# Kernel optimization log

Hardware: AMD Instinct MI355X
Metric: run time of the kernel (lower is better)

The kernel has to match this reference:

```python
import jax, jax.numpy as jnp
import numpy as np

B, T, V, LSRC, D = 4, 128, 50257, 512, 512
PAD_ID = 0
GAMMA1, GAMMA2 = 1.0, 0.1
BETA, MAX_ITER = 2.0, 400


def setup_inputs() -> dict:
    key = jax.random.key(0)
    ks = jax.random.split(key, 7)
    # output_mle are per-token probabilities (original takes torch.log of them)
    output_mle = jax.random.uniform(ks[0], (B, T, V), jnp.float32, 1e-4, 1.0)
    attn_dist = jax.random.uniform(ks[1], (B, LSRC, T), jnp.float32)
    coverage = jax.random.uniform(ks[2], (B, LSRC, T), jnp.float32)
    trg = jax.random.randint(ks[3], (B, T), 0, V)
    dec_mask = jax.random.randint(ks[4], (B, T), 0, 2).astype(bool)
    dec_len = jax.random.randint(ks[5], (B,), 1, T)
    W_emb = jax.random.normal(ks[6], (V, D), jnp.float32) * 0.02
    return {"output_mle": output_mle, "attn_dist": attn_dist, "coverage": coverage,
            "trg": trg, "dec_mask": dec_mask, "dec_len": dec_len, "W_emb": W_emb}


def ipot(a1, a2, beta=BETA, max_iter=MAX_ITER):
    # a1, a2: [n, d_hid] (already flattened from [B, T, d_hid])
    n = a1.shape[0]
    a1n = a1 / jnp.linalg.norm(a1, axis=1, keepdims=True)
    a2n = a2 / jnp.linalg.norm(a2, axis=1, keepdims=True)
    C = a1n @ a2n.T                      # [n, n] cosine cost
    A = jnp.exp(-C / beta)
    eye = jnp.eye(n, dtype=C.dtype)
    sigma0 = jnp.full((n, 1), 1.0 / n, C.dtype)
    T0 = jnp.full((n, n), 1.0 / (n * n), C.dtype)

    def step(carry, _):
        Tm, sigma = carry
        Q = A * Tm
        dvec = 1.0 / n / (Q @ sigma)          # [n, 1]
        sigma = 1.0 / n / (Q.T @ dvec)        # [n, 1]
        # Faithful to torch source: diag(d) * Q * diag(sigma) is ELEMENTWISE,
        # so only the diagonal of the product survives.
        Tm = dvec * Q * sigma.T * eye
        return (Tm, sigma), None

    (Tm, _), _ = jax.lax.scan(step, (T0, sigma0), None, length=max_iter)
    return jnp.sum(Tm * C)


def reference(output_mle, attn_dist, coverage, trg, dec_mask, dec_len, W_emb):
    # --- NLL loss (Eq. 6): mean -log p[target] over non-pad tokens ---
    logp = jnp.log(output_mle)
    tok_lp = jnp.take_along_axis(logp, trg[..., None], axis=-1)[..., 0]   # [B, T]
    valid = (trg != PAD_ID)
    nll = -jnp.sum(jnp.where(valid, tok_lp, 0.0)) / jnp.sum(valid).astype(logp.dtype)

    # --- Coverage loss (Eq. 12) ---
    cov = jnp.sum(jnp.minimum(attn_dist, coverage), axis=1)               # [B, T]
    cov = jnp.where(dec_mask, 0.0, cov)
    cov_loss = jnp.sum(cov) / jnp.sum(dec_len).astype(cov.dtype)

    # --- OT loss via IPOT ---
    trg_emb = W_emb[trg]                                                  # [B, T, D]
    probs = jax.nn.softmax(output_mle, axis=-1)
    pred = jnp.einsum('btv,vd->btd', probs, W_emb)                        # [B, T, D]
    ot = ipot(pred.reshape(-1, D), trg_emb.reshape(-1, D))

    # Faithful to source: gamma2 added as a constant (not multiplied by ot)
    return nll + GAMMA1 * cov_loss + GAMMA2 + ot
```

## Files before the change

### kernel.cpp

```cpp
#include <hip/hip_runtime.h>
#include <math.h>

#define B_ 4
#define T_ 128
#define V_ 50257
#define D_ 512
#define NROWS 512
#define GAMMA2_ 0.1f

#define BK 32
#define KC 1600
#define SPLITK 32
#define NIT (KC / BK)
#define LDA 40
#define LDB 40
#define SLICE (NROWS * D_)
#define WS_PART_OFF 1024

#define SPLITK2 48
#define KC2 1056
#define KP 50688
#define NXB 2048
#define NWB ((KP / 64) * (D_ / 64))
#define ACC_BYTES 4096
#define XB_BYTES ((size_t)NROWS * KP * 2)
#define WT_BYTES ((size_t)D_ * KP * 2)
#define PART2_BYTES ((size_t)SPLITK2 * SLICE * 4)
#define NEED_NEW (ACC_BYTES + XB_BYTES + WT_BYTES + PART2_BYTES)

typedef __attribute__((ext_vector_type(8))) short s8v;
typedef __attribute__((ext_vector_type(4))) float f4v;

__device__ inline unsigned int pack2bf(float f0, float f1) {
    unsigned int u0 = __float_as_uint(f0);
    unsigned int u1 = __float_as_uint(f1);
    u0 += 0x7fffu + ((u0 >> 16) & 1u);
    u1 += 0x7fffu + ((u1 >> 16) & 1u);
    return (u0 >> 16) | (u1 & 0xffff0000u);
}

__device__ inline void sync_lds() {
    __builtin_amdgcn_s_waitcnt(0xC07F);
    __builtin_amdgcn_s_barrier();
}

__device__ inline float wave_reduce(float v) {
    #pragma unroll
    for (int o = 32; o > 0; o >>= 1) v += __shfl_down(v, o, 64);
    return v;
}

__device__ __forceinline__ void gload16(const unsigned short* g, unsigned short* l) {
    __builtin_amdgcn_global_load_lds(
        (const __attribute__((address_space(1))) unsigned int*)g,
        (__attribute__((address_space(3))) unsigned int*)l, 16, 0, 0);
}

__device__ void misc_body(int bid,
                          const float* __restrict__ output_mle,
                          const float* __restrict__ attn,
                          const float* __restrict__ cover,
                          const int* __restrict__ trg,
                          const int* __restrict__ dec_mask,
                          const int* __restrict__ dec_len,
                          float* __restrict__ acc) {
    if (bid < 64) {
        float s = 0.f;
        const float4* a4 = (const float4*)attn;
        const float4* c4 = (const float4*)cover;
        for (int i4 = bid * 256 + threadIdx.x; i4 < 65536; i4 += 64 * 256) {
            float4 a = a4[i4];
            float4 c = c4[i4];
            int b = i4 >> 14;
            int t = (i4 << 2) & (T_ - 1);
            int4 m = *(const int4*)&dec_mask[(b << 7) + t];
            s += m.x ? 0.f : fminf(a.x, c.x);
            s += m.y ? 0.f : fminf(a.y, c.y);
            s += m.z ? 0.f : fminf(a.z, c.z);
            s += m.w ? 0.f : fminf(a.w, c.w);
        }
        s = wave_reduce(s);
        if ((threadIdx.x & 63) == 0) atomicAdd(&acc[2], s);
    } else {
        float lp = 0.f, cnt = 0.f;
        for (int i = threadIdx.x; i < NROWS; i += 256) {
            int tg = trg[i];
            if (tg != 0) {
                lp += __logf(output_mle[(size_t)i * V_ + tg]);
                cnt += 1.f;
            }
        }
        lp = wave_reduce(lp); cnt = wave_reduce(cnt);
        if ((threadIdx.x & 63) == 0) { atomicAdd(&acc[0], lp); atomicAdd(&acc[1], cnt); }
        if (threadIdx.x < B_) atomicAdd(&acc[3], (float)dec_len[threadIdx.x]);
    }
}

__global__ void misc_kernel(const float* __restrict__ output_mle,
                            const float* __restrict__ attn,
                            const float* __restrict__ cover,
                            const int* __restrict__ trg,
                            const int* __restrict__ dec_mask,
                            const int* __restrict__ dec_len,
                            float* __restrict__ acc) {
    misc_body(blockIdx.x, output_mle, attn, cover, trg, dec_mask, dec_len, acc);
}

__launch_bounds__(256)
__global__ void prep_kernel(const float* __restrict__ X,
                            const float* __restrict__ W,
                            const float* __restrict__ attn,
                            const float* __restrict__ cover,
                            const int* __restrict__ trg,
                            const int* __restrict__ dec_mask,
                            const int* __restrict__ dec_len,
                            float* __restrict__ acc,
                            unsigned short* __restrict__ Xb,
                            unsigned short* __restrict__ Wt) {
    const int bid = blockIdx.x;
    const int tid = threadIdx.x;
    if (bid < NXB) {
        const int upr = KP / 8;
        for (int u = bid * 256 + tid; u < NROWS * upr; u += NXB * 256) {
            int row = u / upr;
            int k8  = (u - row * upr) * 8;
            const float* src = X + (size_t)row * V_ + k8;
            unsigned int pk[4];
            if (k8 + 8 <= V_) {
                float e[8];
                #pragma unroll
                for (int j = 0; j < 8; j++) e[j] = __expf(src[j]);
                #pragma unroll
                for (int p = 0; p < 4; p++) pk[p] = pack2bf(e[2 * p], e[2 * p + 1]);
            } else {
                #pragma unroll
                for (int p = 0; p < 4; p++) {
                    float e0 = (k8 + 2 * p     < V_) ? __expf(src[2 * p])     : 0.f;
                    float e1 = (k8 + 2 * p + 1 < V_) ? __expf(src[2 * p + 1]) : 0.f;
                    pk[p] = pack2bf(e0, e1);
                }
            }
            *(uint4*)&Xb[(size_t)row * KP + k8] = *(uint4*)pk;
        }
    } else if (bid < NXB + NWB) {
        __shared__ float Ls[64][64];
        int w  = bid - NXB;
        int kt = w >> 3;
        int dt = w & 7;
        int k0 = kt << 6, d0 = dt << 6;
        int r0 = tid >> 4;
        int c0 = (tid & 15) << 2;
        #pragma unroll
        for (int q = 0; q < 4; q++) {
            int r  = (q << 4) + r0;
            int gk = k0 + r;
            float4 v;
            if (gk < V_) v = *(const float4*)&W[(size_t)gk * D_ + d0 + c0];
            else         v = make_float4(0.f, 0.f, 0.f, 0.f);
            *(float4*)&Ls[r][c0] = v;
        }
        __syncthreads();
        int d  = tid >> 2;
        int kc = (tid & 3) << 4;
        unsigned int pk[8];
        #pragma unroll
        for (int p = 0; p < 8; p++)
            pk[p] = pack2bf(Ls[kc + 2 * p][d], Ls[kc + 2 * p + 1][d]);
        unsigned short* dst = Wt + (size_t)(d0 + d) * KP + k0 + kc;
        *(uint4*)&dst[0] = *(uint4*)&pk[0];
        *(uint4*)&dst[8] = *(uint4*)&pk[4];
    } else {
        misc_body(bid - (NXB + NWB), X, attn, cover, trg, dec_mask, dec_len, acc);
    }
}

__launch_bounds__(256)
__global__ void gemm2_kernel(const unsigned short* __restrict__ Xb,
                             const unsigned short* __restrict__ Wt,
                             float* __restrict__ part) {
    __shared__ __align__(16) unsigned short As[128 * 32];
    __shared__ __align__(16) unsigned short Bs[128 * 32];

    const int bx   = blockIdx.x;
    const int tile = bx & 15;
    const int s    = bx >> 4;
    const int i0   = (tile & 3) * 128;
    const int d0   = (tile >> 2) * 128;
    const size_t ks = (size_t)s * KC2;

    const int tid  = threadIdx.x;
    const int lane = tid & 63;
    const int wave = tid >> 6;
    const int wm   = (wave & 1) * 64;
    const int wn   = (wave >> 1) * 64;
    const int l15  = lane & 15;
    const int l4   = lane >> 4;

    const int grow = wave * 16 + (lane >> 2);
    const int gk8  = (lane & 3) * 8;
    const unsigned short* gA0 = Xb + (size_t)(i0 + grow) * KP + ks + gk8;
    const unsigned short* gA1 = gA0 + (size_t)64 * KP;
    const unsigned short* gB0 = Wt + (size_t)(d0 + grow) * KP + ks + gk8;
    const unsigned short* gB1 = gB0 + (size_t)64 * KP;
    unsigned short* lA = As + wave * 512;
    unsigned short* lB = Bs + wave * 512;

    f4v acc[4][4];
    #pragma unroll
    for (int a = 0; a < 4; a++)
        #pragma unroll
        for (int b = 0; b < 4; b++) acc[a][b] = (f4v)0.f;

    #pragma unroll 1
    for (int kk = 0; kk < KC2; kk += 32) {
        __syncthreads();
        gload16(gA0 + kk, lA);
        gload16(gA1 + kk, lA + 2048);
        gload16(gB0 + kk, lB);
        gload16(gB1 + kk, lB + 2048);
        __syncthreads();
        s8v af[4], bfr[4];
        #pragma unroll
        for (int mi = 0; mi < 4; mi++)
            af[mi] = *(const s8v*)&As[(wm + mi * 16 + l15) * 32 + l4 * 8];
        #pragma unroll
        for (int ni = 0; ni < 4; ni++)
            bfr[ni] = *(const s8v*)&Bs[(wn + ni * 16 + l15) * 32 + l4 * 8];
        #pragma unroll
        for (int mi = 0; mi < 4; mi++)
            #pragma unroll
            for (int ni = 0; ni < 4; ni++)
                acc[mi][ni] = __builtin_amdgcn_mfma_f32_16x16x32_bf16(
                    af[mi], bfr[ni], acc[mi][ni], 0, 0, 0);
    }

    float* dst = part + (size_t)s * SLICE;
    #pragma unroll
    for (int mi = 0; mi < 4; mi++) {
        #pragma unroll
        for (int ni = 0; ni < 4; ni++) {
            int col = d0 + wn + ni * 16 + l15;
            #pragma unroll
            for (int r = 0; r < 4; r++) {
                int row = i0 + wm + mi * 16 + l4 * 4 + r;
                dst[row * D_ + col] = acc[mi][ni][r];
            }
        }
    }
}

__launch_bounds__(256)
__global__ void gemm_kernel(const float* __restrict__ X,
                            const float* __restrict__ W,
                            float* __restrict__ part,
                            int use_atomic) {
    __shared__ __align__(16) short As[128 * LDA];
    __shared__ __align__(16) short Bs[128 * LDB];

    const int bx   = blockIdx.x;
    const int tile = bx & 15;
    const int s    = bx >> 4;
    const int i0   = (tile & 3) * 128;
    const int d0   = (tile >> 2) * 128;
    const int ks   = s * KC;
    const int ke   = min(ks + KC, V_);

    const int tid  = threadIdx.x;
    const int lane = tid & 63;
    const int wave = tid >> 6;
    const int wm   = (wave & 1) * 64;
    const int wn   = (wave >> 1) * 64;
    const int l15  = lane & 15;
    const int l4   = lane >> 4;

    const int ar   = tid >> 1;
    const int akh  = (tid & 1) * 16;
    const int bn2  = (tid & 63) * 2;
    const int bkq  = (tid >> 6) * 8;

    f4v acc[4][4];
    #pragma unroll
    for (int a = 0; a < 4; a++)
        #pragma unroll
        for (int b = 0; b < 4; b++) acc[a][b] = (f4v)0.f;

    auto stageA = [&](const float4 (&ab)[4]) {
        const float* f = (const float*)&ab[0];
        unsigned int au[8];
        #pragma unroll
        for (int p = 0; p < 8; p++)
            au[p] = pack2bf(__expf(f[2 * p]), __expf(f[2 * p + 1]));
        *(uint4*)&As[ar * LDA + akh]     = *(const uint4*)&au[0];
        *(uint4*)&As[ar * LDA + akh + 8] = *(const uint4*)&au[4];
    };
    auto stageB = [&](const float2 (&bb)[8]) {
        unsigned int r0[4], r1[4];
        #pragma unroll
        for (int p = 0; p < 4; p++) {
            r0[p] = pack2bf(bb[2 * p].x, bb[2 * p + 1].x);
            r1[p] = pack2bf(bb[2 * p].y, bb[2 * p + 1].y);
        }
        *(uint4*)&Bs[bn2 * LDB + bkq]       = *(const uint4*)&r0[0];
        *(uint4*)&Bs[(bn2 + 1) * LDB + bkq] = *(const uint4*)&r1[0];
    };
    auto domfma = [&]() {
        s8v af[4], bfr[4];
        #pragma unroll
        for (int mi = 0; mi < 4; mi++)
            af[mi] = *(const s8v*)&As[(wm + mi * 16 + l15) * LDA + l4 * 8];
        #pragma unroll
        for (int ni = 0; ni < 4; ni++)
            bfr[ni] = *(const s8v*)&Bs[(wn + ni * 16 + l15) * LDB + l4 * 8];
        #pragma unroll
        for (int mi = 0; mi < 4; mi++)
            #pragma unroll
            for (int ni = 0; ni < 4; ni++)
                acc[mi][ni] = __builtin_amdgcn_mfma_f32_16x16x32_bf16(
                    af[mi], bfr[ni], acc[mi][ni], 0, 0, 0);
    };
    auto issue = [&](float4 (&ab)[4], float2 (&bb)[8], const float* ap, const float* bp) {
        #pragma unroll
        for (int q = 0; q < 4; q++) ab[q] = *(const float4*)(ap + q * 4);
        #pragma unroll
        for (int j = 0; j < 8; j++) bb[j] = *(const float2*)(bp + (size_t)j * D_);
    };

    if (ks + KC <= V_) {
        const float* ap = X + (size_t)(i0 + ar) * V_ + ks + akh;
        const float* bp = W + d0 + bn2 + (size_t)(ks + bkq) * D_;
        float4 a0[4], a1[4];
        float2 b0[8], b1[8];
        issue(a0, b0, ap, bp);
        #pragma unroll 1
        for (int it = 0; it < NIT; it += 2) {
            ap += BK; bp += (size_t)BK * D_;
            if (it + 1 < NIT) issue(a1, b1, ap, bp);
            sync_lds();
            stageA(a0); stageB(b0);
            sync_lds();
            domfma();

            ap += BK; bp += (size_t)BK * D_;
            if (it + 2 < NIT) issue(a0, b0, ap, bp);
            sync_lds();
            stageA(a1); stageB(b1);
            sync_lds();
            domfma();
        }
    } else {
        const float* Abase = X + (size_t)(i0 + ar) * V_;
        const float* Bbase = W + d0 + bn2;
        for (int k0 = ks; k0 < ke; k0 += BK) {
            float4 ab[4];
            float2 bb[8];
            #pragma unroll
            for (int q = 0; q < 4; q++) {
                int gk = min(k0 + akh + q * 4, V_ - 4);
                ab[q] = *(const float4*)(Abase + gk);
            }
            #pragma unroll
            for (int j = 0; j < 8; j++) {
                int gk = min(k0 + bkq + j, V_ - 1);
                bb[j] = *(const float2*)(Bbase + (size_t)gk * D_);
            }
            sync_lds();
            {
                unsigned int au[8];
                const float* f = (const float*)&ab[0];
                #pragma unroll
                for (int p = 0; p < 8; p++) {
                    int g0 = k0 + akh + 2 * p;
                    float e0 = (g0     < ke) ? __expf(f[2 * p])     : 0.f;
                    float e1 = (g0 + 1 < ke) ? __expf(f[2 * p + 1]) : 0.f;
                    au[p] = pack2bf(e0, e1);
                }
                *(uint4*)&As[ar * LDA + akh]     = *(const uint4*)&au[0];
                *(uint4*)&As[ar * LDA + akh + 8] = *(const uint4*)&au[4];
            }
            {
                unsigned int r0[4], r1[4];
                #pragma unroll
                for (int p = 0; p < 4; p++) {
                    int g0 = k0 + bkq + 2 * p;
                    float x0 = (g0     < ke) ? bb[2 * p].x     : 0.f;
                    float x1 = (g0 + 1 < ke) ? bb[2 * p + 1].x : 0.f;
                    float y0 = (g0     < ke) ? bb[2 * p].y     : 0.f;
                    float y1 = (g0 + 1 < ke) ? bb[2 * p + 1].y : 0.f;
                    r0[p] = pack2bf(x0, x1);
                    r1[p] = pack2bf(y0, y1);
                }
                *(uint4*)&Bs[bn2 * LDB + bkq]       = *(const uint4*)&r0[0];
                *(uint4*)&Bs[(bn2 + 1) * LDB + bkq] = *(const uint4*)&r1[0];
            }
            sync_lds();
            domfma();
        }
    }

    float* dst = part + (use_atomic ? 0 : (size_t)s * SLICE);
    #pragma unroll
    for (int mi = 0; mi < 4; mi++) {
        #pragma unroll
        for (int ni = 0; ni < 4; ni++) {
            int col = d0 + wn + ni * 16 + l15;
            #pragma unroll
            for (int r = 0; r < 4; r++) {
                int row = i0 + wm + mi * 16 + l4 * 4 + r;
                if (use_atomic) atomicAdd(&dst[row * D_ + col], acc[mi][ni][r]);
                else            dst[row * D_ + col] = acc[mi][ni][r];
            }
        }
    }
}

__global__ void ot_kernel(const float* __restrict__ part,
                          const float* __restrict__ W,
                          const int* __restrict__ trg,
                          float* __restrict__ acc,
                          int nsl) {
    int wave = threadIdx.x >> 6, lane = threadIdx.x & 63;
    int row  = blockIdx.x * 4 + wave;
    const size_t off = (size_t)row * D_ + lane * 8;

    float4 p0 = {0, 0, 0, 0}, p1 = {0, 0, 0, 0};
    for (int s = 0; s < nsl; s++) {
        const float4* ps = (const float4*)(part + (size_t)s * SLICE + off);
        float4 q0 = ps[0], q1 = ps[1];
        p0.x += q0.x; p0.y += q0.y; p0.z += q0.z; p0.w += q0.w;
        p1.x += q1.x; p1.y += q1.y; p1.z += q1.z; p1.w += q1.w;
    }
    const float4* t4 = (const float4*)(W + (size_t)trg[row] * D_ + lane * 8);
    float4 t0 = t4[0], t1 = t4[1];

    float dot = p0.x * t0.x + p0.y * t0.y + p0.z * t0.z + p0.w * t0.w
              + p1.x * t1.x + p1.y * t1.y + p1.z * t1.z + p1.w * t1.w;
    float nn  = p0.x * p0.x + p0.y * p0.y + p0.z * p0.z + p0.w * p0.w
              + p1.x * p1.x + p1.y * p1.y + p1.z * p1.z + p1.w * p1.w;
    float tt  = t0.x * t0.x + t0.y * t0.y + t0.z * t0.z + t0.w * t0.w
              + t1.x * t1.x + t1.y * t1.y + t1.z * t1.z + t1.w * t1.w;

    dot = wave_reduce(dot); nn = wave_reduce(nn); tt = wave_reduce(tt);
    if (lane == 0)
        atomicAdd(&acc[4], (dot / sqrtf(nn * tt)) * (1.0f / (float)NROWS));
}

__global__ void finalize_kernel(const float* __restrict__ acc, float* __restrict__ out) {
    if (threadIdx.x == 0)
        out[0] = -acc[0] / acc[1] + acc[2] / acc[3] + GAMMA2_ + acc[4];
}

extern "C" void kernel_launch(void* const* d_in, const int* in_sizes, int n_in,
                              void* d_out, int out_size, void* d_ws, size_t ws_size,
                              hipStream_t stream) {
    const float* output_mle = (const float*)d_in[0];
    const float* attn       = (const float*)d_in[1];
    const float* cover      = (const float*)d_in[2];
    const int*   trg        = (const int*)d_in[3];
    const int*   dec_mask   = (const int*)d_in[4];
    const int*   dec_len    = (const int*)d_in[5];
    const float* W          = (const float*)d_in[6];
    float* out  = (float*)d_out;
    float* acc  = (float*)d_ws;

    const bool newpath = (ws_size >= NEED_NEW);

    if (newpath) {
        unsigned short* Xb = (unsigned short*)((char*)d_ws + ACC_BYTES);
        unsigned short* Wt = (unsigned short*)((char*)d_ws + ACC_BYTES + XB_BYTES);
        float* part2 = (float*)((char*)d_ws + ACC_BYTES + XB_BYTES + WT_BYTES);
        hipMemsetAsync(d_ws, 0, ACC_BYTES, stream);
        prep_kernel<<<NXB + NWB + 65, 256, 0, stream>>>(
            output_mle, W, attn, cover, trg, dec_mask, dec_len, acc, Xb, Wt);
        gemm2_kernel<<<16 * SPLITK2, 256, 0, stream>>>(Xb, Wt, part2);
        ot_kernel<<<NROWS / 4, 256, 0, stream>>>(part2, W, trg, acc, SPLITK2);
        finalize_kernel<<<1, 64, 0, stream>>>(acc, out);
    } else {
        float* part = acc + WS_PART_OFF;
        const size_t need = (size_t)WS_PART_OFF * 4 + (size_t)SPLITK * SLICE * 4;
        const bool partial = (ws_size >= need);
        if (partial) {
            hipMemsetAsync(d_ws, 0, WS_PART_OFF * sizeof(float), stream);
        } else {
            hipMemsetAsync(d_ws, 0, (WS_PART_OFF + SLICE) * sizeof(float), stream);
        }
        misc_kernel<<<65, 256, 0, stream>>>(output_mle, attn, cover, trg, dec_mask, dec_len, acc);
        gemm_kernel<<<16 * SPLITK, 256, 0, stream>>>(output_mle, W, part, partial ? 0 : 1);
        ot_kernel<<<NROWS / 4, 256, 0, stream>>>(part, W, trg, acc, partial ? SPLITK : 1);
        finalize_kernel<<<1, 64, 0, stream>>>(acc, out);
    }
}
```

Baseline: 331.0 us.

## Double-buffer GEMM LDS, vectorize exp conversion, swizzle transpose, parallelize OT reduction

Several independent changes. Each X-conversion block now handles one quarter of a row, using float4 loads and 16 elements per thread. The W transpose tile in LDS gets a rotation swizzle to avoid bank conflicts. The bf16 GEMM double-buffers its LDS tiles so global loads for the next k-step overlap the MFMA work, with one barrier per step. The OT kernel now splits the split-K partial sum across four waves per row and combines them through shared memory, using four times as many blocks. The costs are more LDS per GEMM block and a more complex loop tail.

Result: slower. 340.3 us (+2.8%).

```diff
diff --git a/kernel.cpp b/kernel.cpp
--- a/kernel.cpp
+++ b/kernel.cpp
@@ -21,6 +21,7 @@
 #define KC2 1056
 #define KP 50688
 #define NXB 2048
+#define XUPQ 792
 #define NWB ((KP / 64) * (D_ / 64))
 #define ACC_BYTES 4096
 #define XB_BYTES ((size_t)NROWS * KP * 2)
@@ -120,27 +121,38 @@
     const int bid = blockIdx.x;
     const int tid = threadIdx.x;
     if (bid < NXB) {
-        const int upr = KP / 8;
-        for (int u = bid * 256 + tid; u < NROWS * upr; u += NXB * 256) {
-            int row = u / upr;
-            int k8  = (u - row * upr) * 8;
-            const float* src = X + (size_t)row * V_ + k8;
-            unsigned int pk[4];
-            if (k8 + 8 <= V_) {
-                float e[8];
-                #pragma unroll
-                for (int j = 0; j < 8; j++) e[j] = __expf(src[j]);
-                #pragma unroll
-                for (int p = 0; p < 4; p++) pk[p] = pack2bf(e[2 * p], e[2 * p + 1]);
+        const int row  = bid >> 2;
+        const int q    = bid & 3;
+        const int base = q * XUPQ;
+        const float* src = X + (size_t)row * V_;
+        unsigned short* dst = Xb + (size_t)row * KP;
+        #pragma unroll 2
+        for (int i = tid; i < XUPQ; i += 256) {
+            int k16 = (base + i) << 4;
+            unsigned int pk[8];
+            if (k16 + 16 <= V_) {
+                float4 v0 = *(const float4*)(src + k16);
+                float4 v1 = *(const float4*)(src + k16 + 4);
+                float4 v2 = *(const float4*)(src + k16 + 8);
+                float4 v3 = *(const float4*)(src + k16 + 12);
+                pk[0] = pack2bf(__expf(v0.x), __expf(v0.y));
+                pk[1] = pack2bf(__expf(v0.z), __expf(v0.w));
+                pk[2] = pack2bf(__expf(v1.x), __expf(v1.y));
+                pk[3] = pack2bf(__expf(v1.z), __expf(v1.w));
+                pk[4] = pack2bf(__expf(v2.x), __expf(v2.y));
+                pk[5] = pack2bf(__expf(v2.z), __expf(v2.w));
+                pk[6] = pack2bf(__expf(v3.x), __expf(v3.y));
+                pk[7] = pack2bf(__expf(v3.z), __expf(v3.w));
             } else {
                 #pragma unroll
-                for (int p = 0; p < 4; p++) {
-                    float e0 = (k8 + 2 * p     < V_) ? __expf(src[2 * p])     : 0.f;
-                    float e1 = (k8 + 2 * p + 1 < V_) ? __expf(src[2 * p + 1]) : 0.f;
+                for (int p = 0; p < 8; p++) {
+                    float e0 = (k16 + 2 * p     < V_) ? __expf(src[k16 + 2 * p])     : 0.f;
+                    float e1 = (k16 + 2 * p + 1 < V_) ? __expf(src[k16 + 2 * p + 1]) : 0.f;
                     pk[p] = pack2bf(e0, e1);
                 }
             }
-            *(uint4*)&Xb[(size_t)row * KP + k8] = *(uint4*)pk;
+            *(uint4*)&dst[k16]     = *(uint4*)&pk[0];
+            *(uint4*)&dst[k16 + 8] = *(uint4*)&pk[4];
         }
     } else if (bid < NXB + NWB) {
         __shared__ float Ls[64][64];
@@ -157,16 +169,18 @@
             float4 v;
             if (gk < V_) v = *(const float4*)&W[(size_t)gk * D_ + d0 + c0];
             else         v = make_float4(0.f, 0.f, 0.f, 0.f);
-            *(float4*)&Ls[r][c0] = v;
+            int cr = (c0 + (r & 48)) & 63;
+            *(float4*)&Ls[r][cr] = v;
         }
         __syncthreads();
-        int d  = tid >> 2;
-        int kc = (tid & 3) << 4;
+        int d   = tid >> 2;
+        int rb  = (tid & 3) << 4;
+        int cr  = (d + rb) & 63;
         unsigned int pk[8];
         #pragma unroll
         for (int p = 0; p < 8; p++)
-            pk[p] = pack2bf(Ls[kc + 2 * p][d], Ls[kc + 2 * p + 1][d]);
-        unsigned short* dst = Wt + (size_t)(d0 + d) * KP + k0 + kc;
+            pk[p] = pack2bf(Ls[rb + 2 * p][cr], Ls[rb + 2 * p + 1][cr]);
+        unsigned short* dst = Wt + (size_t)(d0 + d) * KP + k0 + rb;
         *(uint4*)&dst[0] = *(uint4*)&pk[0];
         *(uint4*)&dst[8] = *(uint4*)&pk[4];
     } else {
@@ -178,8 +192,8 @@
 __global__ void gemm2_kernel(const unsigned short* __restrict__ Xb,
                              const unsigned short* __restrict__ Wt,
                              float* __restrict__ part) {
-    __shared__ __align__(16) unsigned short As[128 * 32];
-    __shared__ __align__(16) unsigned short Bs[128 * 32];
+    __shared__ __align__(16) unsigned short As[2][128 * 32];
+    __shared__ __align__(16) unsigned short Bs[2][128 * 32];
 
     const int bx   = blockIdx.x;
     const int tile = bx & 15;
@@ -202,8 +216,6 @@
     const unsigned short* gA1 = gA0 + (size_t)64 * KP;
     const unsigned short* gB0 = Wt + (size_t)(d0 + grow) * KP + ks + gk8;
     const unsigned short* gB1 = gB0 + (size_t)64 * KP;
-    unsigned short* lA = As + wave * 512;
-    unsigned short* lB = Bs + wave * 512;
 
     f4v acc[4][4];
     #pragma unroll
@@ -211,28 +223,40 @@
         #pragma unroll
         for (int b = 0; b < 4; b++) acc[a][b] = (f4v)0.f;
 
-    #pragma unroll 1
-    for (int kk = 0; kk < KC2; kk += 32) {
-        __syncthreads();
-        gload16(gA0 + kk, lA);
-        gload16(gA1 + kk, lA + 2048);
-        gload16(gB0 + kk, lB);
-        gload16(gB1 + kk, lB + 2048);
-        __syncthreads();
+    auto stage = [&](unsigned short* Ab, unsigned short* Bb, int off) {
+        gload16(gA0 + off, Ab + wave * 512);
+        gload16(gA1 + off, Ab + wave * 512 + 2048);
+        gload16(gB0 + off, Bb + wave * 512);
+        gload16(gB1 + off, Bb + wave * 512 + 2048);
+    };
+    auto compute = [&](const unsigned short* Ab, const unsigned short* Bb) {
         s8v af[4], bfr[4];
         #pragma unroll
         for (int mi = 0; mi < 4; mi++)
-            af[mi] = *(const s8v*)&As[(wm + mi * 16 + l15) * 32 + l4 * 8];
+            af[mi] = *(const s8v*)&Ab[(wm + mi * 16 + l15) * 32 + l4 * 8];
         #pragma unroll
         for (int ni = 0; ni < 4; ni++)
-            bfr[ni] = *(const s8v*)&Bs[(wn + ni * 16 + l15) * 32 + l4 * 8];
+            bfr[ni] = *(const s8v*)&Bb[(wn + ni * 16 + l15) * 32 + l4 * 8];
         #pragma unroll
         for (int mi = 0; mi < 4; mi++)
             #pragma unroll
             for (int ni = 0; ni < 4; ni++)
                 acc[mi][ni] = __builtin_amdgcn_mfma_f32_16x16x32_bf16(
                     af[mi], bfr[ni], acc[mi][ni], 0, 0, 0);
-    }
+    };
+
+    stage(As[0], Bs[0], 0);
+    __syncthreads();
+    #pragma unroll 1
+    for (int it = 0; it + 2 < KC2 / 32; it += 2) {
+        stage(As[1], Bs[1], (it + 1) * 32);
+        compute(As[0], Bs[0]);
+        __syncthreads();
+        stage(As[0], Bs[0], (it + 2) * 32);
+        compute(As[1], Bs[1]);
+        __syncthreads();
+    }
+    compute(As[0], Bs[0]);
 
     float* dst = part + (size_t)s * SLICE;
     #pragma unroll
@@ -418,30 +442,44 @@
                           const int* __restrict__ trg,
                           float* __restrict__ acc,
                           int nsl) {
+    __shared__ float Ps[4][D_];
     int wave = threadIdx.x >> 6, lane = threadIdx.x & 63;
-    int row  = blockIdx.x * 4 + wave;
+    int row  = blockIdx.x;
     const size_t off = (size_t)row * D_ + lane * 8;
 
     float4 p0 = {0, 0, 0, 0}, p1 = {0, 0, 0, 0};
-    for (int s = 0; s < nsl; s++) {
+    for (int s = wave; s < nsl; s += 4) {
         const float4* ps = (const float4*)(part + (size_t)s * SLICE + off);
         float4 q0 = ps[0], q1 = ps[1];
         p0.x += q0.x; p0.y += q0.y; p0.z += q0.z; p0.w += q0.w;
         p1.x += q1.x; p1.y += q1.y; p1.z += q1.z; p1.w += q1.w;
     }
-    const float4* t4 = (const float4*)(W + (size_t)trg[row] * D_ + lane * 8);
-    float4 t0 = t4[0], t1 = t4[1];
-
-    float dot = p0.x * t0.x + p0.y * t0.y + p0.z * t0.z + p0.w * t0.w
-              + p1.x * t1.x + p1.y * t1.y + p1.z * t1.z + p1.w * t1.w;
-    float nn  = p0.x * p0.x + p0.y * p0.y + p0.z * p0.z + p0.w * p0.w
-              + p1.x * p1.x + p1.y * p1.y + p1.z * p1.z + p1.w * p1.w;
-    float tt  = t0.x * t0.x + t0.y * t0.y + t0.z * t0.z + t0.w * t0.w
-              + t1.x * t1.x + t1.y * t1.y + t1.z * t1.z + t1.w * t1.w;
-
-    dot = wave_reduce(dot); nn = wave_reduce(nn); tt = wave_reduce(tt);
-    if (lane == 0)
-        atomicAdd(&acc[4], (dot / sqrtf(nn * tt)) * (1.0f / (float)NROWS));
+    *(float4*)&Ps[wave][lane * 8]     = p0;
+    *(float4*)&Ps[wave][lane * 8 + 4] = p1;
+    __syncthreads();
+    if (wave == 0) {
+        float4 s0 = {0, 0, 0, 0}, s1 = {0, 0, 0, 0};
+        #pragma unroll
+        for (int w = 0; w < 4; w++) {
+            float4 q0 = *(const float4*)&Ps[w][lane * 8];
+            float4 q1 = *(const float4*)&Ps[w][lane * 8 + 4];
+            s0.x += q0.x; s0.y += q0.y; s0.z += q0.z; s0.w += q0.w;
+            s1.x += q1.x; s1.y += q1.y; s1.z += q1.z; s1.w += q1.w;
+        }
+        const float4* t4 = (const float4*)(W + (size_t)trg[row] * D_ + lane * 8);
+        float4 t0 = t4[0], t1 = t4[1];
+
+        float dot = s0.x * t0.x + s0.y * t0.y + s0.z * t0.z + s0.w * t0.w
+                  + s1.x * t1.x + s1.y * t1.y + s1.z * t1.z + s1.w * t1.w;
+        float nn  = s0.x * s0.x + s0.y * s0.y + s0.z * s0.z + s0.w * s0.w
+                  + s1.x * s1.x + s1.y * s1.y + s1.z * s1.z + s1.w * s1.w;
+        float tt  = t0.x * t0.x + t0.y * t0.y + t0.z * t0.z + t0.w * t0.w
+                  + t1.x * t1.x + t1.y * t1.y + t1.z * t1.z + t1.w * t1.w;
+
+        dot = wave_reduce(dot); nn = wave_reduce(nn); tt = wave_reduce(tt);
+        if (lane == 0)
+            atomicAdd(&acc[4], (dot / sqrtf(nn * tt)) * (1.0f / (float)NROWS));
+    }
 }
 
 __global__ void finalize_kernel(const float* __restrict__ acc, float* __restrict__ out) {
@@ -472,7 +510,7 @@
         prep_kernel<<<NXB + NWB + 65, 256, 0, stream>>>(
             output_mle, W, attn, cover, trg, dec_mask, dec_len, acc, Xb, Wt);
         gemm2_kernel<<<16 * SPLITK2, 256, 0, stream>>>(Xb, Wt, part2);
-        ot_kernel<<<NROWS / 4, 256, 0, stream>>>(part2, W, trg, acc, SPLITK2);
+        ot_kernel<<<NROWS, 256, 0, stream>>>(part2, W, trg, acc, SPLITK2);
         finalize_kernel<<<1, 64, 0, stream>>>(acc, out);
     } else {
         float* part = acc + WS_PART_OFF;
@@ -485,7 +523,7 @@
         }
         misc_kernel<<<65, 256, 0, stream>>>(output_mle, attn, cover, trg, dec_mask, dec_len, acc);
         gemm_kernel<<<16 * SPLITK, 256, 0, stream>>>(output_mle, W, part, partial ? 0 : 1);
-        ot_kernel<<<NROWS / 4, 256, 0, stream>>>(part, W, trg, acc, partial ? SPLITK : 1);
+        ot_kernel<<<NROWS, 256, 0, stream>>>(part, W, trg, acc, partial ? SPLITK : 1);
         finalize_kernel<<<1, 64, 0, stream>>>(acc, out);
     }
 }
```
